# Performance work log

Measured on AMD Instinct MI355X. Metric: run time of the kernel, lower is better.

The kernel has to match this reference:

```python
import math
import jax, jax.numpy as jnp
import numpy as np


def setup_inputs() -> dict:
    key = jax.random.key(0)
    T, C = 8192, 2048
    layer_depth, num_layers = 5, 10
    ks = jax.random.split(key, 8)

    x = jax.random.normal(ks[0], (T, C), jnp.float32)
    sx = jax.random.normal(ks[1], (C,), jnp.float32)
    aa = jnp.zeros((C,), jnp.float32)
    bb = jnp.zeros((C,), jnp.float32)
    pp = jnp.zeros((C,), jnp.float32)

    # parameter initial values per TimeMix.setup
    r01 = layer_depth / (num_layers - 1)
    r10 = 1.0 - layer_depth / num_layers
    zigzag = 0.5 * (jnp.arange(1, C + 1) % 3 - 1).astype(jnp.float32)
    time_first = jnp.full((C,), math.log(0.3), jnp.float32) + zigzag
    h = jnp.arange(C, dtype=jnp.float32)
    time_decay = (-5.0 + 8.0 * (h / (C - 1)) ** (0.7 + 1.3 * r01)).astype(jnp.float32)
    xr = jnp.arange(C, dtype=jnp.float32) / C
    time_mix_k = xr ** r10
    time_mix_v = time_mix_k + 0.3 * r01
    time_mix_r = xr ** (0.5 * r10)

    ln_scale = jnp.ones((C,), jnp.float32)
    ln_bias = jnp.zeros((C,), jnp.float32)

    s = 1.0 / np.sqrt(C)  # lecun-normal-ish scale for Dense kernels
    Wk = jax.random.normal(ks[2], (C, C), jnp.float32) * s
    Wv = jax.random.normal(ks[3], (C, C), jnp.float32) * s
    Wr = jax.random.normal(ks[4], (C, C), jnp.float32) * s
    Wo = jax.random.normal(ks[5], (C, C), jnp.float32) * s

    return dict(x=x, sx=sx, aa=aa, bb=bb, pp=pp,
                time_first=time_first, time_decay=time_decay,
                time_mix_k=time_mix_k, time_mix_v=time_mix_v, time_mix_r=time_mix_r,
                ln_scale=ln_scale, ln_bias=ln_bias,
                Wk=Wk, Wv=Wv, Wr=Wr, Wo=Wo)


def reference(x, sx, aa, bb, pp, time_first, time_decay,
              time_mix_k, time_mix_v, time_mix_r,
              ln_scale, ln_bias, Wk, Wv, Wr, Wo):
    # LayerNorm(eps=1e-5)
    mu = jnp.mean(x, axis=-1, keepdims=True)
    var = jnp.var(x, axis=-1, keepdims=True)
    xx = (x - mu) * jax.lax.rsqrt(var + 1e-5) * ln_scale + ln_bias  # [T, C]

    # token shift: previous timestep (sx state for t=0)
    sxs = jnp.concatenate((sx[None, :], xx[:-1, :]), axis=0)  # [T, C]
    kx = xx * time_mix_k + sxs * (1.0 - time_mix_k)
    vx = xx * time_mix_v + sxs * (1.0 - time_mix_v)
    rx = xx * time_mix_r + sxs * (1.0 - time_mix_r)

    r = jax.nn.sigmoid(rx @ Wr)  # [T, C]
    k = kx @ Wk                  # [T, C]
    v = vx @ Wv                  # [T, C]

    w = -jnp.exp(time_decay)     # [C]

    def step(state, kv):
        aa, bb, pp = state
        kk, vv = kv
        # output with numerically-stable log-sum-exp style bookkeeping
        ww = time_first + kk
        p = jnp.maximum(pp, ww)
        e1 = jnp.exp(pp - p)
        e2 = jnp.exp(ww - p)
        out = ((e1 * aa + e2 * vv) / (e1 * bb + e2)).astype(r.dtype)
        # state update
        ww2 = w + pp
        p2 = jnp.maximum(ww2, kk)
        e1b = jnp.exp(ww2 - p2)
        e2b = jnp.exp(kk - p2)
        aa = e1b * aa + e2b * vv
        bb = e1b * bb + e2b
        return (aa, bb, p2), out

    (aa, bb, pp), wkv = jax.lax.scan(step, (aa, bb, pp), (k, v))  # wkv: [T, C]

    out = x + (r * wkv) @ Wo
    return (out, xx[-1, :], aa, bb, pp)
```

## Files before the change

### kernel.cpp

```cpp
#include <hip/hip_runtime.h>
#include <stdint.h>

#define T_DIM 8192
#define C_DIM 2048
#define LCHUNK 128
#define NCHUNK (T_DIM / LCHUNK)

typedef unsigned short u16;
typedef __bf16 bf16x8_t __attribute__((ext_vector_type(8)));
typedef float f32x4_t __attribute__((ext_vector_type(4)));

__device__ __forceinline__ u16 f2bf(float f) {
    union { float f; uint32_t u; } x; x.f = f;
    uint32_t r = x.u + 0x7fffu + ((x.u >> 16) & 1u);
    return (u16)(r >> 16);
}
__device__ __forceinline__ float bf2f(u16 u) {
    union { uint32_t u; float f; } x; x.u = ((uint32_t)u) << 16;
    return x.f;
}
__device__ __forceinline__ void gload16(const void* g, void* l) {
    __builtin_amdgcn_global_load_lds((const __attribute__((address_space(1))) uint32_t*)g,
                                     (__attribute__((address_space(3))) uint32_t*)l, 16, 0, 0);
}

__global__ __launch_bounds__(256)
void transpose_cast(const float* __restrict__ W0, const float* __restrict__ W1,
                    const float* __restrict__ W2, const float* __restrict__ W3,
                    u16* __restrict__ Wt)
{
    __shared__ float tile[32][33];
    const int z = blockIdx.z;
    const float* W = (z == 0) ? W0 : (z == 1) ? W1 : (z == 2) ? W2 : W3;
    u16* Tm = Wt + (size_t)z * C_DIM * C_DIM;
    const int tx = threadIdx.x & 31, ty = threadIdx.x >> 5;
    const int bn = blockIdx.x * 32, bk = blockIdx.y * 32;
#pragma unroll
    for (int i = 0; i < 4; ++i)
        tile[ty + 8 * i][tx] = W[(size_t)(bk + ty + 8 * i) * C_DIM + bn + tx];
    __syncthreads();
#pragma unroll
    for (int i = 0; i < 4; ++i)
        Tm[(size_t)(bn + ty + 8 * i) * C_DIM + bk + tx] = f2bf(tile[tx][ty + 8 * i]);
}

union F8 { float4 v[2]; float f[8]; };

__global__ __launch_bounds__(256)
void ln_mix_kernel(const float* __restrict__ x, const float* __restrict__ sx,
                   const float* __restrict__ lns, const float* __restrict__ lnb,
                   const float* __restrict__ tmk, const float* __restrict__ tmv,
                   const float* __restrict__ tmr,
                   u16* __restrict__ kx, u16* __restrict__ vx, u16* __restrict__ rx,
                   float* __restrict__ xx_last)
{
    const int t = blockIdx.x;
    const int tid = threadIdx.x;
    const size_t rowoff = (size_t)t * C_DIM;

    F8 a, p;
    const float4* xt = (const float4*)(x + rowoff);
    a.v[0] = xt[2 * tid]; a.v[1] = xt[2 * tid + 1];
    const float4* xp = (t == 0) ? (const float4*)sx : (const float4*)(x + rowoff - C_DIM);
    p.v[0] = xp[2 * tid]; p.v[1] = xp[2 * tid + 1];

    float s1 = 0.f, s2 = 0.f, s3 = 0.f, s4 = 0.f;
#pragma unroll
    for (int i = 0; i < 8; ++i) {
        s1 += a.f[i]; s2 += a.f[i] * a.f[i];
        s3 += p.f[i]; s4 += p.f[i] * p.f[i];
    }
#pragma unroll
    for (int off = 32; off; off >>= 1) {
        s1 += __shfl_down(s1, off);
        s2 += __shfl_down(s2, off);
        s3 += __shfl_down(s3, off);
        s4 += __shfl_down(s4, off);
    }
    __shared__ float red[4][4];
    if ((tid & 63) == 0) {
        red[0][tid >> 6] = s1; red[1][tid >> 6] = s2;
        red[2][tid >> 6] = s3; red[3][tid >> 6] = s4;
    }
    __syncthreads();
    s1 = red[0][0] + red[0][1] + red[0][2] + red[0][3];
    s2 = red[1][0] + red[1][1] + red[1][2] + red[1][3];
    s3 = red[2][0] + red[2][1] + red[2][2] + red[2][3];
    s4 = red[3][0] + red[3][1] + red[3][2] + red[3][3];
    const float inv = 1.0f / (float)C_DIM;
    const float mu = s1 * inv;
    const float rstd = rsqrtf(s2 * inv - mu * mu + 1e-5f);
    const float mup = s3 * inv;
    const float rstdp = rsqrtf(s4 * inv - mup * mup + 1e-5f);

    F8 ls, lb, mk, mv, mr;
    { const float4* q = (const float4*)lns; ls.v[0] = q[2*tid]; ls.v[1] = q[2*tid+1]; }
    { const float4* q = (const float4*)lnb; lb.v[0] = q[2*tid]; lb.v[1] = q[2*tid+1]; }
    { const float4* q = (const float4*)tmk; mk.v[0] = q[2*tid]; mk.v[1] = q[2*tid+1]; }
    { const float4* q = (const float4*)tmv; mv.v[0] = q[2*tid]; mv.v[1] = q[2*tid+1]; }
    { const float4* q = (const float4*)tmr; mr.v[0] = q[2*tid]; mr.v[1] = q[2*tid+1]; }

    union { u16 u[8]; uint4 q; } ok, ov, orr;
#pragma unroll
    for (int i = 0; i < 8; ++i) {
        const float xxv  = (a.f[i] - mu) * rstd * ls.f[i] + lb.f[i];
        const float prev = (t == 0) ? p.f[i] : (p.f[i] - mup) * rstdp * ls.f[i] + lb.f[i];
        ok.u[i]  = f2bf(xxv * mk.f[i] + prev * (1.f - mk.f[i]));
        ov.u[i]  = f2bf(xxv * mv.f[i] + prev * (1.f - mv.f[i]));
        orr.u[i] = f2bf(xxv * mr.f[i] + prev * (1.f - mr.f[i]));
        if (t == T_DIM - 1) xx_last[tid * 8 + i] = xxv;
    }
    ((uint4*)(kx + rowoff))[tid] = ok.q;
    ((uint4*)(vx + rowoff))[tid] = ov.q;
    ((uint4*)(rx + rowoff))[tid] = orr.q;
}

__global__ __launch_bounds__(512, 1)
void gemm256(const u16* __restrict__ A, const u16* __restrict__ Bt,
             void* __restrict__ Cout, const float* __restrict__ resid,
             const int mode, const int M, const int N, const int K)
{
    __shared__ u16 lds[4 * 16384];
    const int tid = threadIdx.x;
    const int wave = tid >> 6, lane = tid & 63;
    const int nbm = M >> 8;
    const int m0 = (blockIdx.x % nbm) << 8;
    const int n0 = (blockIdx.x / nbm) << 8;
    const int wm = wave >> 2, wn = wave & 3;
    const int fr = lane & 15, fo = lane >> 4;

    f32x4_t acc[8][4] = {};

    const int srow = lane >> 2;
    const int scol = (lane & 3) * 8;
    const u16* gA0 = A + (size_t)(m0 + wave * 16 + srow) * K + scol;
    const u16* gB0 = Bt + (size_t)(n0 + wave * 16 + srow) * K + scol;
    const size_t ginc = (size_t)128 * K;

    auto stageA = [&](int t) {
        const int b = (t & 3) * 16384;
        const u16* g = gA0 + (size_t)t * 32;
        gload16(g,        lds + b + wave * 512);
        gload16(g + ginc, lds + b + wave * 512 + 4096);
    };
    auto stageB = [&](int t) {
        const int b = (t & 3) * 16384 + 8192;
        const u16* g = gB0 + (size_t)t * 32;
        gload16(g,        lds + b + wave * 512);
        gload16(g + ginc, lds + b + wave * 512 + 4096);
    };

    const int NT = K >> 5;
    stageA(0); stageB(0);
    stageA(1); stageB(1);
    asm volatile("s_waitcnt vmcnt(4)" ::: "memory");
    asm volatile("s_barrier" ::: "memory");

    for (int t = 0; t < NT; ++t) {
        const u16* lA = lds + (t & 3) * 16384;
        const u16* lB = lA + 8192;
        bf16x8_t av[4], bv[4];
#pragma unroll
        for (int i = 0; i < 4; ++i)
            av[i] = *(const bf16x8_t*)(lA + (wm * 128 + i * 16 + fr) * 32 + fo * 8);
#pragma unroll
        for (int i = 0; i < 4; ++i)
            bv[i] = *(const bf16x8_t*)(lB + (wn * 64 + i * 16 + fr) * 32 + fo * 8);
        if (t + 2 < NT) stageA(t + 2);
        asm volatile("s_barrier" ::: "memory");
        __builtin_amdgcn_s_setprio(1);
#pragma unroll
        for (int mi = 0; mi < 4; ++mi)
#pragma unroll
            for (int ni = 0; ni < 4; ++ni)
                acc[mi][ni] = __builtin_amdgcn_mfma_f32_16x16x32_bf16(av[mi], bv[ni], acc[mi][ni], 0, 0, 0);
        __builtin_amdgcn_s_setprio(0);
        asm volatile("s_barrier" ::: "memory");
#pragma unroll
        for (int i = 0; i < 4; ++i)
            av[i] = *(const bf16x8_t*)(lA + (wm * 128 + (i + 4) * 16 + fr) * 32 + fo * 8);
        if (t + 2 < NT) stageB(t + 2);
        if (t + 2 < NT)      { asm volatile("s_waitcnt vmcnt(4)" ::: "memory"); }
        else if (t + 1 < NT) { asm volatile("s_waitcnt vmcnt(0)" ::: "memory"); }
        asm volatile("s_barrier" ::: "memory");
        __builtin_amdgcn_s_setprio(1);
#pragma unroll
        for (int mi = 0; mi < 4; ++mi)
#pragma unroll
            for (int ni = 0; ni < 4; ++ni)
                acc[mi + 4][ni] = __builtin_amdgcn_mfma_f32_16x16x32_bf16(av[mi], bv[ni], acc[mi + 4][ni], 0, 0, 0);
        __builtin_amdgcn_s_setprio(0);
        asm volatile("s_barrier" ::: "memory");
    }

    const int r4 = fo * 4;
#pragma unroll
    for (int mi = 0; mi < 8; ++mi) {
#pragma unroll
        for (int ni = 0; ni < 4; ++ni) {
            const int col = n0 + wn * 64 + ni * 16 + fr;
#pragma unroll
            for (int i = 0; i < 4; ++i) {
                const int row = m0 + wm * 128 + mi * 16 + r4 + i;
                float v = acc[mi][ni][i];
                if (resid) v += resid[(size_t)row * N + col];
                if (mode == 0)      ((float*)Cout)[(size_t)row * N + col] = v;
                else if (mode == 1) ((u16*)Cout)[(size_t)row * N + col] = f2bf(v);
                else {
                    const float s = 1.f / (1.f + __expf(-v));
                    ((u16*)Cout)[(size_t)row * N + col] = f2bf(s);
                }
            }
        }
    }
}

__global__ __launch_bounds__(256)
void scan_partial(const float* __restrict__ k, const u16* __restrict__ v,
                  const float* __restrict__ time_decay,
                  float* __restrict__ pA, float* __restrict__ pB, float* __restrict__ pP)
{
    const int c = blockIdx.y * 256 + threadIdx.x;
    const int j = blockIdx.x;
    const float w = -__expf(time_decay[c]);
    float aa = 0.f, bb = 0.f, pp = -1e30f;
    const float* kp = k + (size_t)j * LCHUNK * C_DIM + c;
    const u16*  vp = v + (size_t)j * LCHUNK * C_DIM + c;
#pragma unroll 4
    for (int i = 0; i < LCHUNK; ++i) {
        const float kk = *kp;
        const float vv = bf2f(*vp);
        kp += C_DIM; vp += C_DIM;
        const float ww = w + pp;
        const float p2 = fmaxf(ww, kk);
        const float e1 = __expf(ww - p2);
        const float e2 = __expf(kk - p2);
        aa = e1 * aa + e2 * vv;
        bb = e1 * bb + e2;
        pp = p2;
    }
    const int o = j * C_DIM + c;
    pA[o] = aa; pB[o] = bb; pP[o] = pp;
}

__global__ __launch_bounds__(256)
void scan_combine(const float* __restrict__ pA, const float* __restrict__ pB,
                  const float* __restrict__ pP,
                  const float* __restrict__ aa_in, const float* __restrict__ bb_in,
                  const float* __restrict__ pp_in,
                  const float* __restrict__ time_decay,
                  float* __restrict__ sA, float* __restrict__ sB, float* __restrict__ sP)
{
    const int c = blockIdx.x * 256 + threadIdx.x;
    const float wL = -__expf(time_decay[c]) * (float)LCHUNK;
    float a = aa_in[c], b = bb_in[c], p = pp_in[c];
    for (int j = 0; j < NCHUNK; ++j) {
        const int o = j * C_DIM + c;
        sA[o] = a; sB[o] = b; sP[o] = p;
        const float A = pA[o], B = pB[o], P = pP[o];
        const float pd = p + wL;
        const float q = fmaxf(pd, P);
        const float e1 = __expf(pd - q), e2 = __expf(P - q);
        a = e1 * a + e2 * A;
        b = e1 * b + e2 * B;
        p = q;
    }
}

__global__ __launch_bounds__(256)
void scan_out(const float* __restrict__ k, const u16* __restrict__ v,
              const u16* __restrict__ r,
              const float* __restrict__ time_decay, const float* __restrict__ time_first,
              const float* __restrict__ sA, const float* __restrict__ sB,
              const float* __restrict__ sP,
              u16* __restrict__ arwkv,
              float* __restrict__ aa_out, float* __restrict__ bb_out, float* __restrict__ pp_out)
{
    const int c = blockIdx.y * 256 + threadIdx.x;
    const int j = blockIdx.x;
    const float w = -__expf(time_decay[c]);
    const float u = time_first[c];
    const int so = j * C_DIM + c;
    float aa = sA[so], bb = sB[so], pp = sP[so];
    const size_t base = (size_t)j * LCHUNK * C_DIM + c;
    const float* kp = k + base;
    const u16*  vp = v + base;
    const u16*  rp = r + base;
    u16* op = arwkv + base;
#pragma unroll 4
    for (int i = 0; i < LCHUNK; ++i) {
        const float kk = *kp;
        const float vv = bf2f(*vp);
        const float sr = bf2f(*rp);
        kp += C_DIM; vp += C_DIM; rp += C_DIM;
        const float ww = u + kk;
        const float p = fmaxf(pp, ww);
        const float e1 = __expf(pp - p);
        const float e2 = __expf(ww - p);
        const float out = (e1 * aa + e2 * vv) / (e1 * bb + e2);
        *op = f2bf(sr * out);
        op += C_DIM;
        const float ww2 = w + pp;
        const float p2 = fmaxf(ww2, kk);
        const float f1 = __expf(ww2 - p2);
        const float f2 = __expf(kk - p2);
        aa = f1 * aa + f2 * vv;
        bb = f1 * bb + f2;
        pp = p2;
    }
    if (j == NCHUNK - 1) { aa_out[c] = aa; bb_out[c] = bb; pp_out[c] = pp; }
}

extern "C" void kernel_launch(void* const* d_in, const int* in_sizes, int n_in,
                              void* d_out, int out_size, void* d_ws, size_t ws_size,
                              hipStream_t stream)
{
    (void)in_sizes; (void)n_in; (void)out_size; (void)ws_size;
    const float* x          = (const float*)d_in[0];
    const float* sx         = (const float*)d_in[1];
    const float* aa_in      = (const float*)d_in[2];
    const float* bb_in      = (const float*)d_in[3];
    const float* pp_in      = (const float*)d_in[4];
    const float* time_first = (const float*)d_in[5];
    const float* time_decay = (const float*)d_in[6];
    const float* tmk        = (const float*)d_in[7];
    const float* tmv        = (const float*)d_in[8];
    const float* tmr        = (const float*)d_in[9];
    const float* lns        = (const float*)d_in[10];
    const float* lnb        = (const float*)d_in[11];
    const float* Wk         = (const float*)d_in[12];
    const float* Wv         = (const float*)d_in[13];
    const float* Wr         = (const float*)d_in[14];
    const float* Wo         = (const float*)d_in[15];

    float* out     = (float*)d_out;
    float* xx_last = out + (size_t)T_DIM * C_DIM;
    float* aa_out  = xx_last + C_DIM;
    float* bb_out  = aa_out + C_DIM;
    float* pp_out  = bb_out + C_DIM;

    const size_t TC = (size_t)T_DIM * C_DIM;
    const size_t C2 = (size_t)C_DIM * C_DIM;
    u16* kx    = (u16*)d_ws;
    u16* vx    = kx + TC;
    u16* rx    = vx + TC;
    u16* Wt    = rx + TC;
    float* kbuf = (float*)(Wt + 4 * C2);
    u16* vbuf   = (u16*)(kbuf + TC);
    float* pA   = (float*)(vbuf + TC);
    float* pB   = pA + (size_t)NCHUNK * C_DIM;
    float* pP   = pB + (size_t)NCHUNK * C_DIM;
    float* sA   = pP + (size_t)NCHUNK * C_DIM;
    float* sB   = sA + (size_t)NCHUNK * C_DIM;
    float* sP   = sB + (size_t)NCHUNK * C_DIM;
    u16* rbuf   = kx;
    u16* arwkv  = rx;

    transpose_cast<<<dim3(C_DIM / 32, C_DIM / 32, 4), 256, 0, stream>>>(Wk, Wv, Wr, Wo, Wt);
    ln_mix_kernel<<<T_DIM, 256, 0, stream>>>(x, sx, lns, lnb, tmk, tmv, tmr, kx, vx, rx, xx_last);

    const int NWG = (T_DIM / 256) * (C_DIM / 256);
    gemm256<<<NWG, 512, 0, stream>>>(kx, Wt + 0 * C2, kbuf, nullptr, 0, T_DIM, C_DIM, C_DIM);
    gemm256<<<NWG, 512, 0, stream>>>(vx, Wt + 1 * C2, vbuf, nullptr, 1, T_DIM, C_DIM, C_DIM);
    gemm256<<<NWG, 512, 0, stream>>>(rx, Wt + 2 * C2, rbuf, nullptr, 2, T_DIM, C_DIM, C_DIM);

    scan_partial<<<dim3(NCHUNK, C_DIM / 256), 256, 0, stream>>>(kbuf, vbuf, time_decay, pA, pB, pP);
    scan_combine<<<C_DIM / 256, 256, 0, stream>>>(pA, pB, pP, aa_in, bb_in, pp_in, time_decay, sA, sB, sP);
    scan_out<<<dim3(NCHUNK, C_DIM / 256), 256, 0, stream>>>(kbuf, vbuf, rbuf, time_decay, time_first,
                                                            sA, sB, sP, arwkv, aa_out, bb_out, pp_out);

    gemm256<<<NWG, 512, 0, stream>>>(arwkv, Wt + 3 * C2, out, x, 0, T_DIM, C_DIM, C_DIM);
}
```

Baseline: 483.4 us.

## Restructure GEMM main loop to K=64 tiles with XOR-swizzled LDS and 4-phase schedule

Moves the bf16 GEMM main loop from a 4-deep ring of K=32 stages to a double-buffered K=64 stage, which halves the number of loop iterations and barrier rounds per K step. The LDS layout gets an XOR swizzle on 16-byte chunks so that the fragment reads avoid bank conflicts. Each iteration is split into four MFMA quadrants, with the prefetch loads for tile t+2 spread across the phases. This adds more barriers per iteration and a tighter vmcnt schedule, and the correctness of the swizzle pairing between writes and reads is a risk.

```diff
diff --git a/kernel.cpp b/kernel.cpp
--- a/kernel.cpp
+++ b/kernel.cpp
@@ -22,6 +22,9 @@
 __device__ __forceinline__ void gload16(const void* g, void* l) {
     __builtin_amdgcn_global_load_lds((const __attribute__((address_space(1))) uint32_t*)g,
                                      (__attribute__((address_space(3))) uint32_t*)l, 16, 0, 0);
+}
+__device__ __forceinline__ f32x4_t mfma16(bf16x8_t a, bf16x8_t b, f32x4_t c) {
+    return __builtin_amdgcn_mfma_f32_16x16x32_bf16(a, b, c, 0, 0, 0);
 }
 
 __global__ __launch_bounds__(256)
@@ -120,7 +123,7 @@
              void* __restrict__ Cout, const float* __restrict__ resid,
              const int mode, const int M, const int N, const int K)
 {
-    __shared__ u16 lds[4 * 16384];
+    __shared__ u16 lds[65536];
     const int tid = threadIdx.x;
     const int wave = tid >> 6, lane = tid & 63;
     const int nbm = M >> 8;
@@ -128,68 +131,112 @@
     const int n0 = (blockIdx.x / nbm) << 8;
     const int wm = wave >> 2, wn = wave & 3;
     const int fr = lane & 15, fo = lane >> 4;
+    const int f7 = fr & 7;
+    const int sw0 = (fo ^ f7) * 8;
+    const int sw1 = sw0 ^ 32;
 
     f32x4_t acc[8][4] = {};
 
-    const int srow = lane >> 2;
-    const int scol = (lane & 3) * 8;
-    const u16* gA0 = A + (size_t)(m0 + wave * 16 + srow) * K + scol;
-    const u16* gB0 = Bt + (size_t)(n0 + wave * 16 + srow) * K + scol;
-    const size_t ginc = (size_t)128 * K;
-
-    auto stageA = [&](int t) {
-        const int b = (t & 3) * 16384;
-        const u16* g = gA0 + (size_t)t * 32;
-        gload16(g,        lds + b + wave * 512);
-        gload16(g + ginc, lds + b + wave * 512 + 4096);
+    const int lrow = lane >> 3;
+    const int scol = ((lane & 7) ^ lrow) * 8;
+    const u16* gA = A  + (size_t)(m0 + wave * 8 + lrow) * K + scol;
+    const u16* gB = Bt + (size_t)(n0 + wave * 8 + lrow) * K + scol;
+    const int dA = wave * 512;
+    const int dB = 16384 + wave * 512;
+
+    auto stA = [&](int t, int h) {
+        const int b = (t & 1) * 32768 + h * 8192 + dA;
+        const u16* g = gA + (size_t)(h * 128) * K + (size_t)t * 64;
+        gload16(g,                  lds + b);
+        gload16(g + (size_t)64 * K, lds + b + 4096);
     };
-    auto stageB = [&](int t) {
-        const int b = (t & 3) * 16384 + 8192;
-        const u16* g = gB0 + (size_t)t * 32;
-        gload16(g,        lds + b + wave * 512);
-        gload16(g + ginc, lds + b + wave * 512 + 4096);
+    auto stB = [&](int t, int h) {
+        const int b = (t & 1) * 32768 + h * 8192 + dB;
+        const u16* g = gB + (size_t)(h * 128) * K + (size_t)t * 64;
+        gload16(g,                  lds + b);
+        gload16(g + (size_t)64 * K, lds + b + 4096);
     };
 
-    const int NT = K >> 5;
-    stageA(0); stageB(0);
-    stageA(1); stageB(1);
-    asm volatile("s_waitcnt vmcnt(4)" ::: "memory");
+    const int NT = K >> 6;
+    stB(0, 0); stB(0, 1); stA(0, 0); stA(0, 1);
+    stB(1, 0); stB(1, 1); stA(1, 0); stA(1, 1);
+    asm volatile("s_waitcnt vmcnt(8)" ::: "memory");
     asm volatile("s_barrier" ::: "memory");
 
+    bf16x8_t a[4][2], b[4][2];
     for (int t = 0; t < NT; ++t) {
-        const u16* lA = lds + (t & 3) * 16384;
-        const u16* lB = lA + 8192;
-        bf16x8_t av[4], bv[4];
-#pragma unroll
-        for (int i = 0; i < 4; ++i)
-            av[i] = *(const bf16x8_t*)(lA + (wm * 128 + i * 16 + fr) * 32 + fo * 8);
-#pragma unroll
-        for (int i = 0; i < 4; ++i)
-            bv[i] = *(const bf16x8_t*)(lB + (wn * 64 + i * 16 + fr) * 32 + fo * 8);
-        if (t + 2 < NT) stageA(t + 2);
+        const int bufo = (t & 1) * 32768;
+        const u16* lA = lds + bufo + (wm * 128 + fr) * 64;
+        const u16* lB = lds + bufo + 16384 + (wn * 64 + fr) * 64;
+        const bool pf = (t + 2 < NT);
+#pragma unroll
+        for (int mi = 0; mi < 4; ++mi) {
+            a[mi][0] = *(const bf16x8_t*)(lA + mi * 1024 + sw0);
+            a[mi][1] = *(const bf16x8_t*)(lA + mi * 1024 + sw1);
+        }
+#pragma unroll
+        for (int ni = 0; ni < 2; ++ni) {
+            b[ni][0] = *(const bf16x8_t*)(lB + ni * 1024 + sw0);
+            b[ni][1] = *(const bf16x8_t*)(lB + ni * 1024 + sw1);
+        }
         asm volatile("s_barrier" ::: "memory");
         __builtin_amdgcn_s_setprio(1);
 #pragma unroll
         for (int mi = 0; mi < 4; ++mi)
 #pragma unroll
-            for (int ni = 0; ni < 4; ++ni)
-                acc[mi][ni] = __builtin_amdgcn_mfma_f32_16x16x32_bf16(av[mi], bv[ni], acc[mi][ni], 0, 0, 0);
+            for (int ni = 0; ni < 2; ++ni) {
+                acc[mi][ni] = mfma16(a[mi][0], b[ni][0], acc[mi][ni]);
+                acc[mi][ni] = mfma16(a[mi][1], b[ni][1], acc[mi][ni]);
+            }
         __builtin_amdgcn_s_setprio(0);
         asm volatile("s_barrier" ::: "memory");
 #pragma unroll
-        for (int i = 0; i < 4; ++i)
-            av[i] = *(const bf16x8_t*)(lA + (wm * 128 + (i + 4) * 16 + fr) * 32 + fo * 8);
-        if (t + 2 < NT) stageB(t + 2);
-        if (t + 2 < NT)      { asm volatile("s_waitcnt vmcnt(4)" ::: "memory"); }
-        else if (t + 1 < NT) { asm volatile("s_waitcnt vmcnt(0)" ::: "memory"); }
+        for (int ni = 2; ni < 4; ++ni) {
+            b[ni][0] = *(const bf16x8_t*)(lB + ni * 1024 + sw0);
+            b[ni][1] = *(const bf16x8_t*)(lB + ni * 1024 + sw1);
+        }
         asm volatile("s_barrier" ::: "memory");
         __builtin_amdgcn_s_setprio(1);
 #pragma unroll
         for (int mi = 0; mi < 4; ++mi)
 #pragma unroll
-            for (int ni = 0; ni < 4; ++ni)
-                acc[mi + 4][ni] = __builtin_amdgcn_mfma_f32_16x16x32_bf16(av[mi], bv[ni], acc[mi + 4][ni], 0, 0, 0);
+            for (int ni = 2; ni < 4; ++ni) {
+                acc[mi][ni] = mfma16(a[mi][0], b[ni][0], acc[mi][ni]);
+                acc[mi][ni] = mfma16(a[mi][1], b[ni][1], acc[mi][ni]);
+            }
         __builtin_amdgcn_s_setprio(0);
+        asm volatile("s_barrier" ::: "memory");
+#pragma unroll
+        for (int mi = 0; mi < 4; ++mi) {
+            a[mi][0] = *(const bf16x8_t*)(lA + (mi + 4) * 1024 + sw0);
+            a[mi][1] = *(const bf16x8_t*)(lA + (mi + 4) * 1024 + sw1);
+        }
+        if (pf) stB(t + 2, 0);
+        asm volatile("s_barrier" ::: "memory");
+        __builtin_amdgcn_s_setprio(1);
+#pragma unroll
+        for (int mi = 0; mi < 4; ++mi)
+#pragma unroll
+            for (int ni = 2; ni < 4; ++ni) {
+                acc[mi + 4][ni] = mfma16(a[mi][0], b[ni][0], acc[mi + 4][ni]);
+                acc[mi + 4][ni] = mfma16(a[mi][1], b[ni][1], acc[mi + 4][ni]);
+            }
+        __builtin_amdgcn_s_setprio(0);
+        asm volatile("s_barrier" ::: "memory");
+        if (pf) { stB(t + 2, 1); stA(t + 2, 0); }
+        asm volatile("s_barrier" ::: "memory");
+        __builtin_amdgcn_s_setprio(1);
+#pragma unroll
+        for (int mi = 0; mi < 4; ++mi)
+#pragma unroll
+            for (int ni = 0; ni < 2; ++ni) {
+                acc[mi + 4][ni] = mfma16(a[mi][0], b[ni][0], acc[mi + 4][ni]);
+                acc[mi + 4][ni] = mfma16(a[mi][1], b[ni][1], acc[mi + 4][ni]);
+            }
+        __builtin_amdgcn_s_setprio(0);
+        if (pf) stA(t + 2, 1);
+        if (pf)                  { asm volatile("s_waitcnt vmcnt(8)" ::: "memory"); }
+        else if (t + 1 < NT)     { asm volatile("s_waitcnt vmcnt(0)" ::: "memory"); }
         asm volatile("s_barrier" ::: "memory");
     }
 
```

Result: faster. 467.9 us (-3.2%).

## Replace 256x256 GEMM with 256x128 tile, 2 WGs/CU, swizzled LDS double buffer

Applied to the files above, without the earlier changes.

Switches the bf16 MFMA GEMM from a 512-thread 256x256 tile with four LDS stages to a 256-thread 256x128 tile that runs two workgroups per CU. LDS holds two stages and uses an XOR-swizzled column layout to reduce bank conflicts on fragment reads. The main loop issues the next stage's loads before the MFMAs and drops the split half-step barriers. The aim is to raise occupancy and cut LDS conflicts, at the cost of less operand reuse per tile and a shallower prefetch pipeline.

```diff
diff --git a/kernel.cpp b/kernel.cpp
--- a/kernel.cpp
+++ b/kernel.cpp
@@ -22,6 +22,9 @@
 __device__ __forceinline__ void gload16(const void* g, void* l) {
     __builtin_amdgcn_global_load_lds((const __attribute__((address_space(1))) uint32_t*)g,
                                      (__attribute__((address_space(3))) uint32_t*)l, 16, 0, 0);
+}
+__device__ __forceinline__ f32x4_t mfma16(bf16x8_t a, bf16x8_t b, f32x4_t c) {
+    return __builtin_amdgcn_mfma_f32_16x16x32_bf16(a, b, c, 0, 0, 0);
 }
 
 __global__ __launch_bounds__(256)
@@ -115,81 +118,63 @@
     ((uint4*)(rx + rowoff))[tid] = orr.q;
 }
 
-__global__ __launch_bounds__(512, 1)
-void gemm256(const u16* __restrict__ A, const u16* __restrict__ Bt,
-             void* __restrict__ Cout, const float* __restrict__ resid,
-             const int mode, const int M, const int N, const int K)
-{
-    __shared__ u16 lds[4 * 16384];
+__global__ __launch_bounds__(256, 2)
+void gemm_tile(const u16* __restrict__ A, const u16* __restrict__ Bt,
+               void* __restrict__ Cout, const float* __restrict__ resid,
+               const int mode, const int M, const int N, const int K)
+{
+    __shared__ u16 lds[2 * 12288];
     const int tid = threadIdx.x;
     const int wave = tid >> 6, lane = tid & 63;
     const int nbm = M >> 8;
-    const int m0 = (blockIdx.x % nbm) << 8;
-    const int n0 = (blockIdx.x / nbm) << 8;
-    const int wm = wave >> 2, wn = wave & 3;
+    const int m0 = (int)(blockIdx.x % nbm) << 8;
+    const int n0 = (int)(blockIdx.x / nbm) << 7;
+    const int wm = wave >> 1, wn = wave & 1;
     const int fr = lane & 15, fo = lane >> 4;
+    const int sw = (fo ^ ((fr >> 1) & 3)) * 8;
 
     f32x4_t acc[8][4] = {};
 
-    const int srow = lane >> 2;
-    const int scol = (lane & 3) * 8;
-    const u16* gA0 = A + (size_t)(m0 + wave * 16 + srow) * K + scol;
-    const u16* gB0 = Bt + (size_t)(n0 + wave * 16 + srow) * K + scol;
-    const size_t ginc = (size_t)128 * K;
-
-    auto stageA = [&](int t) {
-        const int b = (t & 3) * 16384;
-        const u16* g = gA0 + (size_t)t * 32;
-        gload16(g,        lds + b + wave * 512);
-        gload16(g + ginc, lds + b + wave * 512 + 4096);
+    const int lrow = lane >> 2;
+    const int scol = ((lane & 3) ^ ((lane >> 3) & 3)) * 8;
+    const u16* gA = A  + (size_t)(m0 + wave * 16 + lrow) * K + scol;
+    const u16* gB = Bt + (size_t)(n0 + wave * 16 + lrow) * K + scol;
+    const int dstw = wave * 512;
+
+    auto stage = [&](int t) {
+        const int b = (t & 1) * 12288;
+        const u16* ga = gA + (size_t)t * 32;
+        const u16* gb = gB + (size_t)t * 32;
+        gload16(ga,                   lds + b + dstw);
+        gload16(ga + (size_t)64 * K,  lds + b + 2048 + dstw);
+        gload16(ga + (size_t)128 * K, lds + b + 4096 + dstw);
+        gload16(ga + (size_t)192 * K, lds + b + 6144 + dstw);
+        gload16(gb,                   lds + b + 8192 + dstw);
+        gload16(gb + (size_t)64 * K,  lds + b + 10240 + dstw);
     };
-    auto stageB = [&](int t) {
-        const int b = (t & 3) * 16384 + 8192;
-        const u16* g = gB0 + (size_t)t * 32;
-        gload16(g,        lds + b + wave * 512);
-        gload16(g + ginc, lds + b + wave * 512 + 4096);
-    };
 
     const int NT = K >> 5;
-    stageA(0); stageB(0);
-    stageA(1); stageB(1);
-    asm volatile("s_waitcnt vmcnt(4)" ::: "memory");
+    stage(0);
+    asm volatile("s_waitcnt vmcnt(0)" ::: "memory");
     asm volatile("s_barrier" ::: "memory");
 
     for (int t = 0; t < NT; ++t) {
-        const u16* lA = lds + (t & 3) * 16384;
-        const u16* lB = lA + 8192;
-        bf16x8_t av[4], bv[4];
-#pragma unroll
-        for (int i = 0; i < 4; ++i)
-            av[i] = *(const bf16x8_t*)(lA + (wm * 128 + i * 16 + fr) * 32 + fo * 8);
-#pragma unroll
-        for (int i = 0; i < 4; ++i)
-            bv[i] = *(const bf16x8_t*)(lB + (wn * 64 + i * 16 + fr) * 32 + fo * 8);
-        if (t + 2 < NT) stageA(t + 2);
-        asm volatile("s_barrier" ::: "memory");
+        if (t + 1 < NT) stage(t + 1);
+        const u16* lA = lds + (t & 1) * 12288 + (wm * 128 + fr) * 32;
+        const u16* lB = lds + (t & 1) * 12288 + 8192 + (wn * 64 + fr) * 32;
+        bf16x8_t a[8], b[4];
+#pragma unroll
+        for (int mi = 0; mi < 8; ++mi) a[mi] = *(const bf16x8_t*)(lA + mi * 512 + sw);
+#pragma unroll
+        for (int ni = 0; ni < 4; ++ni) b[ni] = *(const bf16x8_t*)(lB + ni * 512 + sw);
         __builtin_amdgcn_s_setprio(1);
 #pragma unroll
-        for (int mi = 0; mi < 4; ++mi)
+        for (int mi = 0; mi < 8; ++mi)
 #pragma unroll
             for (int ni = 0; ni < 4; ++ni)
-                acc[mi][ni] = __builtin_amdgcn_mfma_f32_16x16x32_bf16(av[mi], bv[ni], acc[mi][ni], 0, 0, 0);
+                acc[mi][ni] = mfma16(a[mi], b[ni], acc[mi][ni]);
         __builtin_amdgcn_s_setprio(0);
-        asm volatile("s_barrier" ::: "memory");
-#pragma unroll
-        for (int i = 0; i < 4; ++i)
-            av[i] = *(const bf16x8_t*)(lA + (wm * 128 + (i + 4) * 16 + fr) * 32 + fo * 8);
-        if (t + 2 < NT) stageB(t + 2);
-        if (t + 2 < NT)      { asm volatile("s_waitcnt vmcnt(4)" ::: "memory"); }
-        else if (t + 1 < NT) { asm volatile("s_waitcnt vmcnt(0)" ::: "memory"); }
-        asm volatile("s_barrier" ::: "memory");
-        __builtin_amdgcn_s_setprio(1);
-#pragma unroll
-        for (int mi = 0; mi < 4; ++mi)
-#pragma unroll
-            for (int ni = 0; ni < 4; ++ni)
-                acc[mi + 4][ni] = __builtin_amdgcn_mfma_f32_16x16x32_bf16(av[mi], bv[ni], acc[mi + 4][ni], 0, 0, 0);
-        __builtin_amdgcn_s_setprio(0);
+        asm volatile("s_waitcnt vmcnt(0)" ::: "memory");
         asm volatile("s_barrier" ::: "memory");
     }
 
@@ -359,15 +344,15 @@
     transpose_cast<<<dim3(C_DIM / 32, C_DIM / 32, 4), 256, 0, stream>>>(Wk, Wv, Wr, Wo, Wt);
     ln_mix_kernel<<<T_DIM, 256, 0, stream>>>(x, sx, lns, lnb, tmk, tmv, tmr, kx, vx, rx, xx_last);
 
-    const int NWG = (T_DIM / 256) * (C_DIM / 256);
-    gemm256<<<NWG, 512, 0, stream>>>(kx, Wt + 0 * C2, kbuf, nullptr, 0, T_DIM, C_DIM, C_DIM);
-    gemm256<<<NWG, 512, 0, stream>>>(vx, Wt + 1 * C2, vbuf, nullptr, 1, T_DIM, C_DIM, C_DIM);
-    gemm256<<<NWG, 512, 0, stream>>>(rx, Wt + 2 * C2, rbuf, nullptr, 2, T_DIM, C_DIM, C_DIM);
+    const int NWG = (T_DIM / 256) * (C_DIM / 128);
+    gemm_tile<<<NWG, 256, 0, stream>>>(kx, Wt + 0 * C2, kbuf, nullptr, 0, T_DIM, C_DIM, C_DIM);
+    gemm_tile<<<NWG, 256, 0, stream>>>(vx, Wt + 1 * C2, vbuf, nullptr, 1, T_DIM, C_DIM, C_DIM);
+    gemm_tile<<<NWG, 256, 0, stream>>>(rx, Wt + 2 * C2, rbuf, nullptr, 2, T_DIM, C_DIM, C_DIM);
 
     scan_partial<<<dim3(NCHUNK, C_DIM / 256), 256, 0, stream>>>(kbuf, vbuf, time_decay, pA, pB, pP);
     scan_combine<<<C_DIM / 256, 256, 0, stream>>>(pA, pB, pP, aa_in, bb_in, pp_in, time_decay, sA, sB, sP);
     scan_out<<<dim3(NCHUNK, C_DIM / 256), 256, 0, stream>>>(kbuf, vbuf, rbuf, time_decay, time_first,
                                                             sA, sB, sP, arwkv, aa_out, bb_out, pp_out);
 
-    gemm256<<<NWG, 512, 0, stream>>>(arwkv, Wt + 3 * C2, out, x, 0, T_DIM, C_DIM, C_DIM);
-}
+    gemm_tile<<<NWG, 256, 0, stream>>>(arwkv, Wt + 3 * C2, out, x, 0, T_DIM, C_DIM, C_DIM);
+}
```

After: 487.8 us. No clear change (+0.9%).
